# Kernel tuning notes

Measured on AMD Instinct MI355X. Metric: run time of the kernel, lower is better.

The kernel has to match this reference:

```python
import jax, jax.numpy as jnp
import numpy as np

K = 2.0  # Helmholtz wavenumber (init kwarg k, cast to complex)
N_INT, N_BC, LAT, HID = 262144, 65536, 64, 128


def setup_inputs() -> dict:
    key = jax.random.key(0)
    ks = jax.random.split(key, 10)
    d_in = 3 + LAT
    return {
        "coords_int": jax.random.normal(ks[0], (N_INT, 3), jnp.float32),
        "coords_bc": jax.random.normal(ks[1], (N_BC, 3), jnp.float32),
        "gt_bc": jax.random.normal(ks[2], (N_BC, 1), jnp.float32),
        "latent": jax.random.normal(ks[3], (LAT,), jnp.float32),
        "W1": jax.random.normal(ks[4], (d_in, HID), jnp.float32) / np.sqrt(d_in),
        "b1": jnp.zeros((HID,), jnp.float32),
        "W2": jax.random.normal(ks[5], (HID, HID), jnp.float32) / np.sqrt(HID),
        "b2": jnp.zeros((HID,), jnp.float32),
        "W3": jax.random.normal(ks[6], (HID, 2), jnp.float32) / np.sqrt(HID),
        "b3": jnp.zeros((2,), jnp.float32),
    }


def reference(coords_int, coords_bc, gt_bc, latent, W1, b1, W2, b2, W3, b3):
    k2 = jnp.asarray(complex(K, 0.0) ** 2, jnp.complex64)

    def dec_point(x):  # x: (3,) -> (2,) = (Re p, Im p)
        h = jnp.concatenate([x, latent])
        h = jnp.tanh(h @ W1 + b1)
        h = jnp.tanh(h @ W2 + b2)
        return h @ W3 + b3

    # interior prediction and Hessian diagonal -> Laplacian (per point, vmapped)
    pred_int = jax.vmap(dec_point)(coords_int)               # (N, 2)
    hess = jax.vmap(jax.hessian(dec_point))(coords_int)      # (N, 2, 3, 3)
    lap = jnp.trace(hess, axis1=-2, axis2=-1)                # (N, 2)

    p_c = pred_int[:, 0] + 1j * pred_int[:, 1]
    lap_c = lap[:, 0] + 1j * lap[:, 1]
    helm_res = lap_c + k2 * p_c                              # (N,) complex64
    loss_pde = jnp.mean(helm_res.real ** 2 + helm_res.imag ** 2)

    # boundary branch (batched MLP, latent broadcast)
    hb = jnp.concatenate(
        [coords_bc, jnp.broadcast_to(latent, (coords_bc.shape[0], LAT))], axis=-1
    )
    hb = jnp.tanh(hb @ W1 + b1)
    hb = jnp.tanh(hb @ W2 + b2)
    pred_bc = hb @ W3 + b3                                   # (Nb, 2)
    # gt_bc is real cast to complex -> imag target is 0
    dr = pred_bc[:, 0] - gt_bc[:, 0]
    di = pred_bc[:, 1]
    loss_bc = jnp.mean(dr ** 2 + di ** 2)

    return loss_pde, loss_bc, jax.lax.stop_gradient(helm_res)
```

## Files before the change

### kernel.cpp

```cpp
#include <hip/hip_runtime.h>


#define N_INT 262144
#define N_BC  65536
#define HID   128
#define GRID  512
#define WPB   4
#define NWAVE (GRID * WPB)
#define TILES_INT (N_INT / 16)
#define TILES_BC  (N_BC / 16)
#define TILES_ALL (TILES_INT + TILES_BC)

typedef _Float16 h8 __attribute__((ext_vector_type(8)));
typedef float    f4 __attribute__((ext_vector_type(4)));

__device__ __forceinline__ float ftanh(float x) {
    float e = __expf(2.0f * x);
    return 1.0f - 2.0f * __builtin_amdgcn_rcpf(e + 1.0f);
}

extern "C" __global__ void pde_prep(const float* __restrict__ latent,
                                    const float* __restrict__ W1,
                                    const float* __restrict__ b1,
                                    const float* __restrict__ W2,
                                    const float* __restrict__ b2,
                                    const float* __restrict__ W3,
                                    _Float16* __restrict__ wsB,
                                    float* __restrict__ wsF)
{
    const int tid = threadIdx.x;
    for (int e = 0; e < 64; ++e) {
        int idx = e * 256 + tid;
        int j = idx >> 7, n = idx & 127;
        int s = j >> 5, qd = (j >> 3) & 3, i = j & 7;
        int c = n >> 4,  nn = n & 15;
        wsB[(((s * 8 + c) * 64) + (qd * 16 + nn)) * 8 + i] = (_Float16)W2[idx];
    }
    {
        int col = tid >> 1, h = tid & 1;
        float acc = 0.0f;
        #pragma unroll
        for (int l = 0; l < 32; ++l)
            acc = fmaf(latent[32 * h + l], W1[(3 + 32 * h + l) * HID + col], acc);
        acc += __shfl_xor(acc, 1);
        if (h == 0) wsF[4 * col + 3] = acc + b1[col];
    }
    if (tid < HID) {
        float wx = W1[tid], wy = W1[HID + tid], wz = W1[2 * HID + tid];
        wsF[4 * tid]     = wx;
        wsF[4 * tid + 1] = wy;
        wsF[4 * tid + 2] = wz;
        wsF[512 + tid] = -2.0f * fmaf(wx, wx, fmaf(wy, wy, wz * wz));
        wsF[640 + tid] = b2[tid];
        wsF[768 + 2 * tid]     = W3[2 * tid];
        wsF[768 + 2 * tid + 1] = W3[2 * tid + 1];
    }
}

extern "C" __global__ __launch_bounds__(256, 2)
void pde_mfma(const float* __restrict__ ci, const float* __restrict__ cb,
              const float* __restrict__ gt, const float* __restrict__ b3,
              const _Float16* __restrict__ wsB, const float* __restrict__ wsF,
              float* __restrict__ out)
{
    __shared__ float4 sBv[2048];
    __shared__ float4 sFv[256];
    _Float16* sB = (_Float16*)sBv;
    const float*  sF  = (const float*)sFv;
    const float4* sP  = (const float4*)sF;
    const float*  sQ2 = sF + 512;
    const float*  sB2 = sF + 640;
    const float2* sW3 = (const float2*)(sF + 768);

    const int tid = threadIdx.x;

    #pragma unroll
    for (int e = 0; e < 8; ++e)
        sBv[e * 256 + tid] = ((const float4*)wsB)[e * 256 + tid];
    sFv[tid] = ((const float4*)wsF)[tid];
    __syncthreads();

    const int lane = tid & 63;
    const int m    = lane & 15;
    const int qd   = lane >> 4;
    const int wgid = blockIdx.x * WPB + (tid >> 6);
    const float b30 = b3[0], b31 = b3[1];
    const f4 z4 = {0.0f, 0.0f, 0.0f, 0.0f};

    float lsum = 0.0f, bsum = 0.0f;

    int t = wgid;
    const float* cp0 = (t < TILES_INT) ? (ci + 3 * (t * 16 + m))
                                       : (cb + 3 * ((t - TILES_INT) * 16 + m));
    float x = cp0[0], y = cp0[1], z = cp0[2];

    for (; t < TILES_ALL; t += NWAVE) {
      float nx, ny, nz;
      {
        int tn = t + NWAVE;
        if (tn < TILES_ALL) {
            const float* np = (tn < TILES_INT) ? (ci + 3 * (tn * 16 + m))
                                               : (cb + 3 * ((tn - TILES_INT) * 16 + m));
            nx = np[0]; ny = np[1]; nz = np[2];
        } else { nx = ny = nz = 0.0f; }
      }

      if (t < TILES_INT) {
        const int p0 = t * 16;

        h8 FH[4], FX[4], FY[4], FZ[4], FT[4];
        #pragma unroll
        for (int s = 0; s < 4; ++s) {
            const int j0 = s * 32 + qd * 8;
            #pragma unroll
            for (int i = 0; i < 8; ++i) {
                const int j = j0 + i;
                float4 P = sP[j];
                float z1 = fmaf(x, P.x, fmaf(y, P.y, fmaf(z, P.z, P.w)));
                float h  = ftanh(z1);
                float d  = fmaf(-h, h, 1.0f);
                FH[s][i] = (_Float16)h;
                FX[s][i] = (_Float16)(d * P.x);
                FY[s][i] = (_Float16)(d * P.y);
                FZ[s][i] = (_Float16)(d * P.z);
                FT[s][i] = (_Float16)(sQ2[j] * h * d);
            }
        }

        float yr[4] = {0,0,0,0}, yi[4] = {0,0,0,0};
        float lr[4] = {0,0,0,0}, li[4] = {0,0,0,0};
        #pragma unroll
        for (int c = 0; c < 8; ++c) {
            f4 aZ = z4, aX = z4, aY = z4, aW = z4, aT = z4;
            #pragma unroll
            for (int s = 0; s < 4; ++s) {
                h8 bf = *(const h8*)&sB[(((s * 8 + c) * 64) + lane) * 8];
                aZ = __builtin_amdgcn_mfma_f32_16x16x32_f16(FH[s], bf, aZ, 0, 0, 0);
                aX = __builtin_amdgcn_mfma_f32_16x16x32_f16(FX[s], bf, aX, 0, 0, 0);
                aY = __builtin_amdgcn_mfma_f32_16x16x32_f16(FY[s], bf, aY, 0, 0, 0);
                aW = __builtin_amdgcn_mfma_f32_16x16x32_f16(FZ[s], bf, aW, 0, 0, 0);
                aT = __builtin_amdgcn_mfma_f32_16x16x32_f16(FT[s], bf, aT, 0, 0, 0);
            }
            const int k = c * 16 + m;
            const float b2k = sB2[k];
            const float2 w3 = sW3[k];
            #pragma unroll
            for (int r = 0; r < 4; ++r) {
                float h2 = ftanh(aZ[r] + b2k);
                float d2 = fmaf(-h2, h2, 1.0f);
                float uu = fmaf(aX[r], aX[r], fmaf(aY[r], aY[r], aW[r] * aW[r]));
                float lk = d2 * fmaf(-2.0f * h2, uu, aT[r]);
                yr[r] = fmaf(h2, w3.x, yr[r]);
                yi[r] = fmaf(h2, w3.y, yi[r]);
                lr[r] = fmaf(lk, w3.x, lr[r]);
                li[r] = fmaf(lk, w3.y, li[r]);
            }
        }
        #pragma unroll
        for (int off = 1; off <= 8; off <<= 1) {
            #pragma unroll
            for (int r = 0; r < 4; ++r) {
                yr[r] += __shfl_xor(yr[r], off);
                yi[r] += __shfl_xor(yi[r], off);
                lr[r] += __shfl_xor(lr[r], off);
                li[r] += __shfl_xor(li[r], off);
            }
        }
        if (m == 0) {
            #pragma unroll
            for (int r = 0; r < 4; ++r) {
                float re = fmaf(4.0f, yr[r] + b30, lr[r]);
                float im = fmaf(4.0f, yi[r] + b31, li[r]);
                out[2 + p0 + qd * 4 + r] = re;
                lsum = fmaf(re, re, fmaf(im, im, lsum));
            }
        }
      } else {
        const int q0 = (t - TILES_INT) * 16;

        h8 FH[4];
        #pragma unroll
        for (int s = 0; s < 4; ++s) {
            const int j0 = s * 32 + qd * 8;
            #pragma unroll
            for (int i = 0; i < 8; ++i) {
                const int j = j0 + i;
                float4 P = sP[j];
                float z1 = fmaf(x, P.x, fmaf(y, P.y, fmaf(z, P.z, P.w)));
                FH[s][i] = (_Float16)ftanh(z1);
            }
        }

        float yr[4] = {0,0,0,0}, yi[4] = {0,0,0,0};
        #pragma unroll
        for (int c = 0; c < 8; ++c) {
            f4 aZ = z4;
            #pragma unroll
            for (int s = 0; s < 4; ++s) {
                h8 bf = *(const h8*)&sB[(((s * 8 + c) * 64) + lane) * 8];
                aZ = __builtin_amdgcn_mfma_f32_16x16x32_f16(FH[s], bf, aZ, 0, 0, 0);
            }
            const int k = c * 16 + m;
            const float b2k = sB2[k];
            const float2 w3 = sW3[k];
            #pragma unroll
            for (int r = 0; r < 4; ++r) {
                float h2 = ftanh(aZ[r] + b2k);
                yr[r] = fmaf(h2, w3.x, yr[r]);
                yi[r] = fmaf(h2, w3.y, yi[r]);
            }
        }
        #pragma unroll
        for (int off = 1; off <= 8; off <<= 1) {
            #pragma unroll
            for (int r = 0; r < 4; ++r) {
                yr[r] += __shfl_xor(yr[r], off);
                yi[r] += __shfl_xor(yi[r], off);
            }
        }
        if (m == 0) {
            #pragma unroll
            for (int r = 0; r < 4; ++r) {
                float dr = yr[r] + b30 - gt[q0 + qd * 4 + r];
                float di = yi[r] + b31;
                bsum = fmaf(dr, dr, fmaf(di, di, bsum));
            }
        }
      }

      x = nx; y = ny; z = nz;
    }

    #pragma unroll
    for (int off = 1; off < 64; off <<= 1) {
        lsum += __shfl_xor(lsum, off);
        bsum += __shfl_xor(bsum, off);
    }
    if (lane == 0) {
        atomicAdd(out,     lsum * (1.0f / (float)N_INT));
        atomicAdd(out + 1, bsum * (1.0f / (float)N_BC));
    }
}

extern "C" void kernel_launch(void* const* d_in, const int* in_sizes, int n_in,
                              void* d_out, int out_size, void* d_ws, size_t ws_size,
                              hipStream_t stream)
{
    const float* ci  = (const float*)d_in[0];
    const float* cb  = (const float*)d_in[1];
    const float* gt  = (const float*)d_in[2];
    const float* lat = (const float*)d_in[3];
    const float* W1  = (const float*)d_in[4];
    const float* b1  = (const float*)d_in[5];
    const float* W2  = (const float*)d_in[6];
    const float* b2  = (const float*)d_in[7];
    const float* W3  = (const float*)d_in[8];
    const float* b3  = (const float*)d_in[9];
    float* out = (float*)d_out;

    _Float16* wsB = (_Float16*)d_ws;
    float*    wsF = (float*)((char*)d_ws + 32768);

    hipMemsetAsync(d_out, 0, 2 * sizeof(float), stream);

    hipLaunchKernelGGL(pde_prep, dim3(1), dim3(256), 0, stream,
                       lat, W1, b1, W2, b2, W3, wsB, wsF);
    hipLaunchKernelGGL(pde_mfma, dim3(GRID), dim3(256), 0, stream,
                       ci, cb, gt, b3, wsB, wsF, out);
}
```

Baseline: 195.9 us.

## Interleave layer-1 feature generation with MFMA by keeping all output accumulators live

Reorders the interior and boundary MLP loops so each 32-wide K-slice of layer-1 features is computed and immediately consumed by MFMAs into 8 column-block accumulators. Previously all features were built first, then each column block ran its MFMAs. This lets tanh/VALU work for the next slice overlap with matrix ops, and the fp16 feature arrays no longer need to stay live. In exchange it holds 40 f4 accumulators (160 VGPRs) in the interior path, which raises register pressure and may lower occupancy or cause spills.

```diff
diff --git a/kernel.cpp b/kernel.cpp
--- a/kernel.cpp
+++ b/kernel.cpp
@@ -108,10 +108,14 @@
       if (t < TILES_INT) {
         const int p0 = t * 16;
 
-        h8 FH[4], FX[4], FY[4], FZ[4], FT[4];
+        f4 aZ[8], aX[8], aY[8], aW[8], aT[8];
+        #pragma unroll
+        for (int c = 0; c < 8; ++c) { aZ[c]=z4; aX[c]=z4; aY[c]=z4; aW[c]=z4; aT[c]=z4; }
+
         #pragma unroll
         for (int s = 0; s < 4; ++s) {
             const int j0 = s * 32 + qd * 8;
+            h8 fh, fx, fy, fz, ft;
             #pragma unroll
             for (int i = 0; i < 8; ++i) {
                 const int j = j0 + i;
@@ -119,11 +123,20 @@
                 float z1 = fmaf(x, P.x, fmaf(y, P.y, fmaf(z, P.z, P.w)));
                 float h  = ftanh(z1);
                 float d  = fmaf(-h, h, 1.0f);
-                FH[s][i] = (_Float16)h;
-                FX[s][i] = (_Float16)(d * P.x);
-                FY[s][i] = (_Float16)(d * P.y);
-                FZ[s][i] = (_Float16)(d * P.z);
-                FT[s][i] = (_Float16)(sQ2[j] * h * d);
+                fh[i] = (_Float16)h;
+                fx[i] = (_Float16)(d * P.x);
+                fy[i] = (_Float16)(d * P.y);
+                fz[i] = (_Float16)(d * P.z);
+                ft[i] = (_Float16)(sQ2[j] * h * d);
+            }
+            #pragma unroll
+            for (int c = 0; c < 8; ++c) {
+                h8 bf = *(const h8*)&sB[(((s * 8 + c) * 64) + lane) * 8];
+                aZ[c] = __builtin_amdgcn_mfma_f32_16x16x32_f16(fh, bf, aZ[c], 0, 0, 0);
+                aX[c] = __builtin_amdgcn_mfma_f32_16x16x32_f16(fx, bf, aX[c], 0, 0, 0);
+                aY[c] = __builtin_amdgcn_mfma_f32_16x16x32_f16(fy, bf, aY[c], 0, 0, 0);
+                aW[c] = __builtin_amdgcn_mfma_f32_16x16x32_f16(fz, bf, aW[c], 0, 0, 0);
+                aT[c] = __builtin_amdgcn_mfma_f32_16x16x32_f16(ft, bf, aT[c], 0, 0, 0);
             }
         }
 
@@ -131,25 +144,16 @@
         float lr[4] = {0,0,0,0}, li[4] = {0,0,0,0};
         #pragma unroll
         for (int c = 0; c < 8; ++c) {
-            f4 aZ = z4, aX = z4, aY = z4, aW = z4, aT = z4;
-            #pragma unroll
-            for (int s = 0; s < 4; ++s) {
-                h8 bf = *(const h8*)&sB[(((s * 8 + c) * 64) + lane) * 8];
-                aZ = __builtin_amdgcn_mfma_f32_16x16x32_f16(FH[s], bf, aZ, 0, 0, 0);
-                aX = __builtin_amdgcn_mfma_f32_16x16x32_f16(FX[s], bf, aX, 0, 0, 0);
-                aY = __builtin_amdgcn_mfma_f32_16x16x32_f16(FY[s], bf, aY, 0, 0, 0);
-                aW = __builtin_amdgcn_mfma_f32_16x16x32_f16(FZ[s], bf, aW, 0, 0, 0);
-                aT = __builtin_amdgcn_mfma_f32_16x16x32_f16(FT[s], bf, aT, 0, 0, 0);
-            }
             const int k = c * 16 + m;
             const float b2k = sB2[k];
             const float2 w3 = sW3[k];
             #pragma unroll
             for (int r = 0; r < 4; ++r) {
-                float h2 = ftanh(aZ[r] + b2k);
+                float h2 = ftanh(aZ[c][r] + b2k);
                 float d2 = fmaf(-h2, h2, 1.0f);
-                float uu = fmaf(aX[r], aX[r], fmaf(aY[r], aY[r], aW[r] * aW[r]));
-                float lk = d2 * fmaf(-2.0f * h2, uu, aT[r]);
+                float uu = fmaf(aX[c][r], aX[c][r],
+                            fmaf(aY[c][r], aY[c][r], aW[c][r] * aW[c][r]));
+                float lk = d2 * fmaf(-2.0f * h2, uu, aT[c][r]);
                 yr[r] = fmaf(h2, w3.x, yr[r]);
                 yi[r] = fmaf(h2, w3.y, yi[r]);
                 lr[r] = fmaf(lk, w3.x, lr[r]);
@@ -178,34 +182,37 @@
       } else {
         const int q0 = (t - TILES_INT) * 16;
 
-        h8 FH[4];
+        f4 bZ[8];
+        #pragma unroll
+        for (int c = 0; c < 8; ++c) bZ[c] = z4;
+
         #pragma unroll
         for (int s = 0; s < 4; ++s) {
             const int j0 = s * 32 + qd * 8;
+            h8 fh;
             #pragma unroll
             for (int i = 0; i < 8; ++i) {
                 const int j = j0 + i;
                 float4 P = sP[j];
                 float z1 = fmaf(x, P.x, fmaf(y, P.y, fmaf(z, P.z, P.w)));
-                FH[s][i] = (_Float16)ftanh(z1);
+                fh[i] = (_Float16)ftanh(z1);
+            }
+            #pragma unroll
+            for (int c = 0; c < 8; ++c) {
+                h8 bf = *(const h8*)&sB[(((s * 8 + c) * 64) + lane) * 8];
+                bZ[c] = __builtin_amdgcn_mfma_f32_16x16x32_f16(fh, bf, bZ[c], 0, 0, 0);
             }
         }
 
         float yr[4] = {0,0,0,0}, yi[4] = {0,0,0,0};
         #pragma unroll
         for (int c = 0; c < 8; ++c) {
-            f4 aZ = z4;
-            #pragma unroll
-            for (int s = 0; s < 4; ++s) {
-                h8 bf = *(const h8*)&sB[(((s * 8 + c) * 64) + lane) * 8];
-                aZ = __builtin_amdgcn_mfma_f32_16x16x32_f16(FH[s], bf, aZ, 0, 0, 0);
-            }
             const int k = c * 16 + m;
             const float b2k = sB2[k];
             const float2 w3 = sW3[k];
             #pragma unroll
             for (int r = 0; r < 4; ++r) {
-                float h2 = ftanh(aZ[r] + b2k);
+                float h2 = ftanh(bZ[c][r] + b2k);
                 yr[r] = fmaf(h2, w3.x, yr[r]);
                 yi[r] = fmaf(h2, w3.y, yi[r]);
             }
```

Result: no change. 198.9 us (+1.6%).
